# Performance work log

Hardware: AMD Instinct MI355X
Metric: run time of the kernel (lower is better)

Reference implementation:

```python
import jax, jax.numpy as jnp
import numpy as np
from jax import lax

TOP_K = 6
NORM_MIN = 1e-12


def setup_inputs() -> dict:
    key = jax.random.key(0)
    k0, k1, k2, k3, k4, k5 = jax.random.split(key, 6)
    B, S, H, E, I = 2, 1024, 2048, 64, 512
    return {
        "hidden_states": jax.random.normal(k0, (B, S, H), dtype=jnp.float32),
        "gate_w": jax.random.normal(k1, (E, H), dtype=jnp.float32) * 0.02,
        "e_bias": jax.random.normal(k2, (E,), dtype=jnp.float32) * 0.01,
        "gate_proj": jax.random.normal(k3, (E, H, I), dtype=jnp.float32) * 0.02,
        "up_proj": jax.random.normal(k4, (E, H, I), dtype=jnp.float32) * 0.02,
        "down_proj": jax.random.normal(k5, (E, I, H), dtype=jnp.float32) * 0.02,
    }


def reference(hidden_states, gate_w, e_bias, gate_proj, up_proj, down_proj):
    B, S, H = hidden_states.shape
    E = gate_w.shape[0]
    x = hidden_states.reshape(-1, H)                      # [T, H]
    T = x.shape[0]

    # --- routing (done in float32 in the original) ---
    router_logits = x.astype(jnp.float32) @ gate_w.T      # [T, E]
    routing_probs = jax.nn.softmax(router_logits, axis=-1)
    # topk over bias-corrected scores, but weights come from raw probs
    _, selected = lax.top_k(routing_probs + e_bias[None, :], TOP_K)  # [T, k]
    w = jnp.take_along_axis(routing_probs, selected, axis=-1)        # [T, k]
    w = w / jnp.clip(w.sum(axis=-1, keepdims=True), NORM_MIN)
    w = w.astype(hidden_states.dtype)

    # combine weights: [T, E], zero for unselected experts
    combine = jnp.zeros((T, E), dtype=hidden_states.dtype)
    combine = combine.at[jnp.arange(T)[:, None], selected].add(w)

    # --- experts: SwiGLU MLP per expert, weighted-sum combine ---
    def step(acc, params):
        wg, wu, wd, c = params                            # wg,wu [H,I]; wd [I,H]; c [T]
        h = jax.nn.silu(x @ wg) * (x @ wu)                # [T, I]
        return acc + (h @ wd) * c[:, None], None

    init = jnp.zeros((T, H), dtype=hidden_states.dtype)
    final, _ = lax.scan(step, init, (gate_proj, up_proj, down_proj, combine.T))
    return final.reshape(-1), router_logits.reshape(-1)
```

## Files before the change

kernel.cpp:

```cpp
#include <hip/hip_runtime.h>
#include <math.h>

#define T_TOK 2048
#define H_DIM 2048
#define E_NUM 64
#define I_DIM 512
#define TOPK  6
#define NPAIR (T_TOK * TOPK)
#define MAXTILES 80

typedef __attribute__((ext_vector_type(8))) short s8;
typedef __attribute__((ext_vector_type(4))) float f4;
typedef __attribute__((ext_vector_type(8))) unsigned short u16x8;

static __device__ __forceinline__ unsigned short f2bf(float f) {
  unsigned int u = __float_as_uint(f);
  u += 0x7fff + ((u >> 16) & 1);
  return (unsigned short)(u >> 16);
}
static __device__ __forceinline__ unsigned int cvt_pk(float lo, float hi) {
  unsigned int r;
  asm("v_cvt_pk_bf16_f32 %0, %1, %2" : "=v"(r) : "v"(lo), "v"(hi));
  return r;
}
static __device__ __forceinline__ void gload_lds16(const void* g, void* l) {
  __builtin_amdgcn_global_load_lds(
      (const __attribute__((address_space(1))) unsigned int*)g,
      (__attribute__((address_space(3))) unsigned int*)l, 16, 0, 0);
}
#define SBAR()      __builtin_amdgcn_s_barrier()
#define SCHED0()    __builtin_amdgcn_sched_barrier(0)
#define WAIT_LGKM0() asm volatile("s_waitcnt lgkmcnt(0)" ::: "memory")
#define WAIT_VM0()   asm volatile("s_waitcnt vmcnt(0)" ::: "memory")
#define WAIT_VM2()   asm volatile("s_waitcnt vmcnt(2)" ::: "memory")
#define WAIT_VM4()   asm volatile("s_waitcnt vmcnt(4)" ::: "memory")
#define WAIT_VM6()   asm volatile("s_waitcnt vmcnt(6)" ::: "memory")

__global__ __launch_bounds__(512) void router_kernel(
    const float* __restrict__ x, const float* __restrict__ gw,
    const float* __restrict__ ebias, float* __restrict__ logits_out,
    int* __restrict__ sel, float* __restrict__ wsel)
{
  __shared__ float xs[4][H_DIM];
  __shared__ float lg[4][E_NUM];
  int t0 = blockIdx.x * 4;
  int tid = threadIdx.x;
  {
    float4* xsv = (float4*)&xs[0][0];
    const float4* src = (const float4*)(x + (size_t)t0 * H_DIM);
    for (int i = tid; i < 4 * H_DIM / 4; i += 512) xsv[i] = src[i];
  }
  __syncthreads();

  int wave = tid >> 6, lane = tid & 63;
  for (int ii = 0; ii < 4; ++ii) {
    int e0 = wave * 8 + ii * 2, e1 = e0 + 1;
    const float4* g0 = (const float4*)(gw + (size_t)e0 * H_DIM);
    const float4* g1 = (const float4*)(gw + (size_t)e1 * H_DIM);
    float s00=0.f,s01=0.f,s02=0.f,s03=0.f, s10=0.f,s11=0.f,s12=0.f,s13=0.f;
    for (int h4 = lane; h4 < H_DIM / 4; h4 += 64) {
      float4 w0 = g0[h4], w1 = g1[h4];
      float4 a0 = ((const float4*)xs[0])[h4];
      float4 a1 = ((const float4*)xs[1])[h4];
      float4 a2 = ((const float4*)xs[2])[h4];
      float4 a3 = ((const float4*)xs[3])[h4];
      s00 += w0.x*a0.x + w0.y*a0.y + w0.z*a0.z + w0.w*a0.w;
      s01 += w0.x*a1.x + w0.y*a1.y + w0.z*a1.z + w0.w*a1.w;
      s02 += w0.x*a2.x + w0.y*a2.y + w0.z*a2.z + w0.w*a2.w;
      s03 += w0.x*a3.x + w0.y*a3.y + w0.z*a3.z + w0.w*a3.w;
      s10 += w1.x*a0.x + w1.y*a0.y + w1.z*a0.z + w1.w*a0.w;
      s11 += w1.x*a1.x + w1.y*a1.y + w1.z*a1.z + w1.w*a1.w;
      s12 += w1.x*a2.x + w1.y*a2.y + w1.z*a2.z + w1.w*a2.w;
      s13 += w1.x*a3.x + w1.y*a3.y + w1.z*a3.z + w1.w*a3.w;
    }
    for (int off = 32; off; off >>= 1) {
      s00 += __shfl_down(s00, off); s01 += __shfl_down(s01, off);
      s02 += __shfl_down(s02, off); s03 += __shfl_down(s03, off);
      s10 += __shfl_down(s10, off); s11 += __shfl_down(s11, off);
      s12 += __shfl_down(s12, off); s13 += __shfl_down(s13, off);
    }
    if (lane == 0) {
      lg[0][e0]=s00; lg[1][e0]=s01; lg[2][e0]=s02; lg[3][e0]=s03;
      lg[0][e1]=s10; lg[1][e1]=s11; lg[2][e1]=s12; lg[3][e1]=s13;
    }
  }
  __syncthreads();

  if (tid < 256) {
    int tt = tid >> 6, e = tid & 63;
    logits_out[(size_t)(t0 + tt) * E_NUM + e] = lg[tt][e];
  }

  if (wave == 0) {
    for (int tt = 0; tt < 4; ++tt) {
      int t = t0 + tt;
      float v = lg[tt][lane];
      float m = v;
      for (int off = 32; off; off >>= 1) m = fmaxf(m, __shfl_xor(m, off));
      float ex = __expf(v - m);
      float sum = ex;
      for (int off = 32; off; off >>= 1) sum += __shfl_xor(sum, off);
      float prob = ex / sum;
      float sc = prob + ebias[lane];

      int selidx[TOPK]; float selw[TOPK]; float wsum = 0.f;
      #pragma unroll
      for (int k = 0; k < TOPK; ++k) {
        float mm = sc;
        for (int off = 32; off; off >>= 1) mm = fmaxf(mm, __shfl_xor(mm, off));
        unsigned long long ball = __ballot(sc == mm);
        int s = __ffsll(ball) - 1;
        float p = __shfl(prob, s);
        selidx[k] = s; selw[k] = p; wsum += p;
        if (lane == s) sc = -INFINITY;
      }
      if (lane == 0) {
        float inv = 1.f / fmaxf(wsum, 1e-12f);
        #pragma unroll
        for (int k = 0; k < TOPK; ++k) {
          sel[t * TOPK + k] = selidx[k];
          wsel[t * TOPK + k] = selw[k] * inv;
        }
      }
    }
  }
}

__global__ __launch_bounds__(64) void build_lists(
    const int* __restrict__ sel, const float* __restrict__ wsel,
    int* __restrict__ cnt, int* __restrict__ toklist, float* __restrict__ wtlist)
{
  int e = blockIdx.x, lane = threadIdx.x;
  int base = 0;
  for (int t0 = 0; t0 < T_TOK; t0 += 64) {
    int t = t0 + lane;
    int flag = 0; float w = 0.f;
    #pragma unroll
    for (int k = 0; k < TOPK; ++k)
      if (sel[t * TOPK + k] == e) { flag = 1; w = wsel[t * TOPK + k]; }
    unsigned long long b = __ballot(flag);
    int pos = base + __popcll(b & ((1ull << lane) - 1ull));
    if (flag) { toklist[e * T_TOK + pos] = t; wtlist[e * T_TOK + pos] = w; }
    base += __popcll(b);
  }
  if (lane == 0) cnt[e] = base;
}

__global__ void scan_kernel(const int* __restrict__ cnt,
                            int* __restrict__ tmap, int* __restrict__ ntile) {
  if (threadIdx.x == 0) {
    int nt = 0;
    for (int e = 0; e < E_NUM; ++e) {
      int m = (cnt[e] + 255) >> 8;
      for (int tb = 0; tb < m && nt < MAXTILES; ++tb) tmap[nt++] = e * 16 + tb;
    }
    *ntile = nt;
  }
}

__global__ __launch_bounds__(256) void permute_kernel(
    const float* __restrict__ x, const int* __restrict__ cnt,
    const int* __restrict__ toklist, const int* __restrict__ tmap,
    const int* __restrict__ ntile, unsigned short* __restrict__ xt)
{
  int tile = blockIdx.y;
  if (tile >= *ntile) return;
  int ks = blockIdx.x;
  int em = tmap[tile], e = em >> 4, tb = em & 15;
  int n = cnt[e];
  int r = threadIdx.x;
  int tok = toklist[e * T_TOK + min(tb * 256 + r, n - 1)];
  const float4* src = (const float4*)(x + (size_t)tok * H_DIM + ks * 32);
  float4 v[8];
  #pragma unroll
  for (int q = 0; q < 8; ++q) v[q] = src[q];
  int g = (r >> 1) & 3;
  unsigned short* dst = xt + ((size_t)(tile * 64 + ks) * 1024 + r * 4) * 8;
  #pragma unroll
  for (int u = 0; u < 4; ++u) {
    int k16 = u ^ g;
    float4 a = v[2 * k16], b = v[2 * k16 + 1];
    u16x8 p;
    ((unsigned int*)&p)[0] = cvt_pk(a.x, a.y);
    ((unsigned int*)&p)[1] = cvt_pk(a.z, a.w);
    ((unsigned int*)&p)[2] = cvt_pk(b.x, b.y);
    ((unsigned int*)&p)[3] = cvt_pk(b.z, b.w);
    *(u16x8*)(dst + u * 8) = p;
  }
}

__global__ __launch_bounds__(512, 4) void gateup_kernel(
    const unsigned short* __restrict__ xt, const float* __restrict__ gp,
    const float* __restrict__ up, const int* __restrict__ tmap,
    const int* __restrict__ ntile, unsigned short* __restrict__ hat)
{
  __shared__ __align__(16) unsigned short A_lds[2][8192];
  __shared__ __align__(16) unsigned int   Bt[2][2][64 * 20];
  int tile = blockIdx.x;
  if (tile >= *ntile) return;
  int e = tmap[tile] >> 4;
  int ic = blockIdx.y, colbase = ic * 64;
  int tid = threadIdx.x, lane = tid & 63, wave = tid >> 6;
  int matc = wave >> 2, cw = wave & 3;
  int lrow = (lane >> 4) * 4, lcol = lane & 15, kgl = lane >> 4;
  int hp = tid & 15, cb = (tid >> 4) & 15, mstage = tid >> 8;
  const float* bsrc0 = ((mstage == 0) ? gp : up)
      + (size_t)e * (H_DIM * I_DIM) + colbase + (size_t)(2 * hp) * I_DIM + cb * 4;
  const unsigned short* achunk0 = xt + (size_t)tile * 64 * 1024 * 8;

  f4 acc[4][4];
  #pragma unroll
  for (int a = 0; a < 4; ++a)
    #pragma unroll
    for (int b = 0; b < 4; ++b) acc[a][b] = (f4)0.f;

  float4 p0, p1, q0, q1;
  {
    const unsigned short* s = achunk0 + (size_t)(wave * 128 + lane) * 8;
    gload_lds16(s,       &A_lds[0][(wave * 128) * 8]);
    gload_lds16(s + 512, &A_lds[0][(wave * 128 + 64) * 8]);
    p0 = *(const float4*)bsrc0;
    p1 = *(const float4*)(bsrc0 + I_DIM);
    WAIT_VM0();
    unsigned int* db = &Bt[0][mstage][cb * 4 * 20 + hp];
    db[0]  = cvt_pk(p0.x, p1.x); db[20] = cvt_pk(p0.y, p1.y);
    db[40] = cvt_pk(p0.z, p1.z); db[60] = cvt_pk(p0.w, p1.w);
    const float* b1 = bsrc0 + (size_t)32 * I_DIM;
    q0 = *(const float4*)b1;
    q1 = *(const float4*)(b1 + I_DIM);
    WAIT_LGKM0();
    SBAR();
    SCHED0();
  }

#define GU_STEP(K, C0, C1, N0, N1) do {                                            \
    if ((K) + 1 < 64) {                                                            \
      const unsigned short* s = achunk0 + ((size_t)((K) + 1) * 1024 + wave * 128 + lane) * 8; \
      gload_lds16(s,       &A_lds[((K) + 1) & 1][(wave * 128) * 8]);               \
      gload_lds16(s + 512, &A_lds[((K) + 1) & 1][(wave * 128 + 64) * 8]);          \
    }                                                                              \
    if ((K) + 2 < 64) {                                                            \
      const float* b = bsrc0 + (size_t)((K) + 2) * 32 * I_DIM;                     \
      N0 = *(const float4*)b; N1 = *(const float4*)(b + I_DIM);                    \
    }                                                                              \
    if ((K) + 2 < 64)      { WAIT_VM4(); }                                         \
    else if ((K) + 1 < 64) { WAIT_VM2(); }                                         \
    else                   { WAIT_VM0(); }                                         \
    if ((K) + 1 < 64) {                                                            \
      unsigned int* db = &Bt[((K) + 1) & 1][mstage][cb * 4 * 20 + hp];             \
      db[0]  = cvt_pk(C0.x, C1.x); db[20] = cvt_pk(C0.y, C1.y);                    \
      db[40] = cvt_pk(C0.z, C1.z); db[60] = cvt_pk(C0.w, C1.w);                    \
    }                                                                              \
    {                                                                              \
      s8 afr[4];                                                                   \
      _Pragma("unroll")                                                            \
      for (int mf = 0; mf < 4; ++mf) {                                             \
        int r = cw * 64 + mf * 16 + lcol;                                          \
        afr[mf] = *(s8*)&A_lds[(K) & 1][r * 32 + ((kgl ^ ((r >> 1) & 3)) * 8)];    \
      }                                                                            \
      _Pragma("unroll")                                                            \
      for (int nf = 0; nf < 4; ++nf) {                                             \
        s8 bfr = *(s8*)&Bt[(K) & 1][matc][(nf * 16 + lcol) * 20 + kgl * 4];        \
        _Pragma("unroll")                                                          \
        for (int mf = 0; mf < 4; ++mf)                                             \
          acc[mf][nf] = __builtin_amdgcn_mfma_f32_16x16x32_bf16(afr[mf], bfr, acc[mf][nf], 0, 0, 0); \
      }                                                                            \
    }                                                                              \
    if ((K) + 1 < 64) {                                                            \
      if ((K) + 2 < 64) { WAIT_VM2(); } else { WAIT_VM0(); }                       \
      WAIT_LGKM0(); SBAR(); SCHED0();                                              \
    }                                                                              \
  } while (0)

  for (int k = 0; k < 64; k += 2) {
    GU_STEP(k,     q0, q1, p0, p1);
    GU_STEP(k + 1, p0, p1, q0, q1);
  }
#undef GU_STEP

  f4* exch = (f4*)&Bt[0][0][0];
  unsigned short* hs = &A_lds[0][0];
  #pragma unroll
  for (int nf = 0; nf < 4; ++nf) {
    __syncthreads();
    if (wave >= 4) {
      #pragma unroll
      for (int mf = 0; mf < 4; ++mf)
        exch[((wave - 4) * 4 + mf) * 64 + lane] = acc[mf][nf];
    }
    __syncthreads();
    if (wave < 4) {
      #pragma unroll
      for (int mf = 0; mf < 4; ++mf) {
        f4 u = exch[(wave * 4 + mf) * 64 + lane];
        #pragma unroll
        for (int j = 0; j < 4; ++j) {
          float g = acc[mf][nf][j];
          float h = g / (1.f + __expf(-g)) * u[j];
          hs[(wave * 64 + mf * 16 + lrow + j) * 64 + nf * 16 + lcol] = f2bf(h);
        }
      }
    }
  }
  __syncthreads();
  #pragma unroll
  for (int c = 0; c < 2; ++c) {
    unsigned short* base = hat + (size_t)(tile * 16 + ic * 2 + c) * 1024 * 8;
    for (int uu = tid; uu < 1024; uu += 512) {
      int row = uu >> 2, k16 = (uu & 3) ^ ((row >> 1) & 3);
      *(u16x8*)(base + (size_t)uu * 8) = *(const u16x8*)&hs[row * 64 + c * 32 + k16 * 8];
    }
  }
}

__global__ __launch_bounds__(256, 4) void down_kernel(
    const unsigned short* __restrict__ hat, const float* __restrict__ dp,
    const int* __restrict__ cnt, const int* __restrict__ tmap,
    const int* __restrict__ ntile, const int* __restrict__ toklist,
    const float* __restrict__ wtlist, float* __restrict__ out)
{
  __shared__ __align__(16) unsigned short A_lds[2][8192];
  __shared__ __align__(16) unsigned int   Bt[2][64 * 20];
  __shared__ int   stok[256];
  __shared__ float swt[256];
  int tile = blockIdx.x;
  if (tile >= *ntile) return;
  int em = tmap[tile], e = em >> 4, tb = em & 15;
  int n = cnt[e];
  int hc = blockIdx.y, colbase = hc * 64;
  int tid = threadIdx.x, lane = tid & 63, wave = tid >> 6, wbase = wave * 64;
  int lrow = (lane >> 4) * 4, lcol = lane & 15, kgl = lane >> 4;
  int hp = tid & 15, cb = tid >> 4;
  const float* bsrc0 = dp + (size_t)e * (I_DIM * H_DIM) + colbase
                       + (size_t)(2 * hp) * H_DIM + cb * 4;
  const unsigned short* achunk0 = hat + (size_t)tile * 16 * 1024 * 8;

  int rr = tb * 256 + tid;
  stok[tid] = (rr < n) ? toklist[e * T_TOK + rr] : 0;
  swt[tid]  = (rr < n) ? wtlist[e * T_TOK + rr] : 0.f;

  f4 acc[4][4];
  #pragma unroll
  for (int a = 0; a < 4; ++a)
    #pragma unroll
    for (int b = 0; b < 4; ++b) acc[a][b] = (f4)0.f;

  float4 p0, p1, q0, q1;
  {
    const unsigned short* s = achunk0 + (size_t)(wave * 256 + lane) * 8;
    #pragma unroll
    for (int i = 0; i < 4; ++i)
      gload_lds16(s + i * 512, &A_lds[0][(wave * 256 + i * 64) * 8]);
    p0 = *(const float4*)bsrc0;
    p1 = *(const float4*)(bsrc0 + H_DIM);
    WAIT_VM0();
    unsigned int* db = &Bt[0][cb * 4 * 20 + hp];
    db[0]  = cvt_pk(p0.x, p1.x); db[20] = cvt_pk(p0.y, p1.y);
    db[40] = cvt_pk(p0.z, p1.z); db[60] = cvt_pk(p0.w, p1.w);
    const float* b1 = bsrc0 + (size_t)32 * H_DIM;
    q0 = *(const float4*)b1;
    q1 = *(const float4*)(b1 + H_DIM);
    WAIT_LGKM0();
    SBAR();
    SCHED0();
  }

#define DN_STEP(K, C0, C1, N0, N1) do {                                            \
    if ((K) + 1 < 16) {                                                            \
      const unsigned short* s = achunk0 + ((size_t)((K) + 1) * 1024 + wave * 256 + lane) * 8; \
      _Pragma("unroll")                                                            \
      for (int i = 0; i < 4; ++i)                                                  \
        gload_lds16(s + i * 512, &A_lds[((K) + 1) & 1][(wave * 256 + i * 64) * 8]);\
    }                                                                              \
    if ((K) + 2 < 16) {                                                            \
      const float* b = bsrc0 + (size_t)((K) + 2) * 32 * H_DIM;                     \
      N0 = *(const float4*)b; N1 = *(const float4*)(b + H_DIM);                    \
    }                                                                              \
    if ((K) + 2 < 16)      { WAIT_VM6(); }                                         \
    else if ((K) + 1 < 16) { WAIT_VM4(); }                                         \
    else                   { WAIT_VM0(); }                                         \
    if ((K) + 1 < 16) {                                                            \
      unsigned int* db = &Bt[((K) + 1) & 1][cb * 4 * 20 + hp];                     \
      db[0]  = cvt_pk(C0.x, C1.x); db[20] = cvt_pk(C0.y, C1.y);                    \
      db[40] = cvt_pk(C0.z, C1.z); db[60] = cvt_pk(C0.w, C1.w);                    \
    }                                                                              \
    {                                                                              \
      s8 afr[4];                                                                   \
      _Pragma("unroll")                                                            \
      for (int mf = 0; mf < 4; ++mf) {                                             \
        int r = wbase + mf * 16 + lcol;                                            \
        afr[mf] = *(s8*)&A_lds[(K) & 1][r * 32 + ((kgl ^ ((r >> 1) & 3)) * 8)];    \
      }                                                                            \
      _Pragma("unroll")                                                            \
      for (int nf = 0; nf < 4; ++nf) {                                             \
        s8 bfr = *(s8*)&Bt[(K) & 1][(nf * 16 + lcol) * 20 + kgl * 4];              \
        _Pragma("unroll")                                                          \
        for (int mf = 0; mf < 4; ++mf)                                             \
          acc[mf][nf] = __builtin_amdgcn_mfma_f32_16x16x32_bf16(afr[mf], bfr, acc[mf][nf], 0, 0, 0); \
      }                                                                            \
    }                                                                              \
    if ((K) + 1 < 16) {                                                            \
      if ((K) + 2 < 16) { WAIT_VM2(); } else { WAIT_VM0(); }                       \
      WAIT_LGKM0(); SBAR(); SCHED0();                                              \
    }                                                                              \
  } while (0)

  for (int k = 0; k < 16; k += 2) {
    DN_STEP(k,     q0, q1, p0, p1);
    DN_STEP(k + 1, p0, p1, q0, q1);
  }
#undef DN_STEP

  #pragma unroll
  for (int mf = 0; mf < 4; ++mf)
    #pragma unroll
    for (int nf = 0; nf < 4; ++nf)
      #pragma unroll
      for (int j = 0; j < 4; ++j) {
        int r = wbase + mf * 16 + lrow + j;
        if (tb * 256 + r < n)
          atomicAdd(&out[(size_t)stok[r] * H_DIM + colbase + nf * 16 + lcol],
                    acc[mf][nf][j] * swt[r]);
      }
}

extern "C" void kernel_launch(void* const* d_in, const int* in_sizes, int n_in,
                              void* d_out, int out_size, void* d_ws, size_t ws_size,
                              hipStream_t stream) {
  const float* hidden = (const float*)d_in[0];
  const float* gate_w = (const float*)d_in[1];
  const float* e_bias = (const float*)d_in[2];
  const float* gate_p = (const float*)d_in[3];
  const float* up_p   = (const float*)d_in[4];
  const float* down_p = (const float*)d_in[5];

  float* out_final  = (float*)d_out;
  float* out_logits = out_final + (size_t)T_TOK * H_DIM;

  int*   cnt     = (int*)d_ws;
  int*   texp    = cnt + 64;
  int*   ntile   = texp + 64;
  int*   tmap    = ntile + 16;
  int*   sel     = tmap + MAXTILES;
  float* wsel    = (float*)(sel + NPAIR);
  int*   toklist = (int*)(wsel + NPAIR);
  float* wtlist  = (float*)(toklist + E_NUM * T_TOK);
  unsigned short* xt  = (unsigned short*)(wtlist + E_NUM * T_TOK);
  unsigned short* hat = xt + (size_t)MAXTILES * 64 * 1024 * 8;

  hipMemsetAsync(out_final, 0, (size_t)T_TOK * H_DIM * sizeof(float), stream);

  router_kernel<<<T_TOK / 4, 512, 0, stream>>>(hidden, gate_w, e_bias, out_logits, sel, wsel);
  build_lists<<<E_NUM, 64, 0, stream>>>(sel, wsel, cnt, toklist, wtlist);
  scan_kernel<<<1, 64, 0, stream>>>(cnt, tmap, ntile);
  permute_kernel<<<dim3(64, MAXTILES), 256, 0, stream>>>(hidden, cnt, toklist, tmap, ntile, xt);
  gateup_kernel<<<dim3(MAXTILES, I_DIM / 64), 512, 0, stream>>>(
      xt, gate_p, up_p, tmap, ntile, hat);
  down_kernel<<<dim3(MAXTILES, H_DIM / 64), 256, 0, stream>>>(
      hat, down_p, cnt, tmap, ntile, toklist, wtlist, out_final);
}
```

Measured before the change: 569.4 us.

## Replace atomic scatter-add in down projection with bf16 partials plus gather-reduce

The down kernel now writes weighted per-(token,expert) results as bf16 rows into a partial buffer (reusing the xt workspace) instead of atomically adding fp32 values into the output. A new reduce kernel gathers each token's six partial rows through a position map built during list construction and writes the output directly, so the output memset is no longer needed. This removes contended global atomics and replaces them with coalesced stores and one extra kernel. In exchange, the partial results are rounded to bf16 before they are summed, which costs some accuracy.

```diff
diff --git a/kernel.cpp b/kernel.cpp
--- a/kernel.cpp
+++ b/kernel.cpp
@@ -128,29 +128,35 @@
 
 __global__ __launch_bounds__(64) void build_lists(
     const int* __restrict__ sel, const float* __restrict__ wsel,
-    int* __restrict__ cnt, int* __restrict__ toklist, float* __restrict__ wtlist)
+    int* __restrict__ cnt, int* __restrict__ toklist, float* __restrict__ wtlist,
+    int* __restrict__ posmap)
 {
   int e = blockIdx.x, lane = threadIdx.x;
   int base = 0;
   for (int t0 = 0; t0 < T_TOK; t0 += 64) {
     int t = t0 + lane;
-    int flag = 0; float w = 0.f;
+    int flag = 0, kk = 0; float w = 0.f;
     #pragma unroll
     for (int k = 0; k < TOPK; ++k)
-      if (sel[t * TOPK + k] == e) { flag = 1; w = wsel[t * TOPK + k]; }
+      if (sel[t * TOPK + k] == e) { flag = 1; kk = k; w = wsel[t * TOPK + k]; }
     unsigned long long b = __ballot(flag);
     int pos = base + __popcll(b & ((1ull << lane) - 1ull));
-    if (flag) { toklist[e * T_TOK + pos] = t; wtlist[e * T_TOK + pos] = w; }
+    if (flag) {
+      toklist[e * T_TOK + pos] = t;
+      wtlist[e * T_TOK + pos] = w;
+      posmap[t * TOPK + kk] = pos;
+    }
     base += __popcll(b);
   }
   if (lane == 0) cnt[e] = base;
 }
 
-__global__ void scan_kernel(const int* __restrict__ cnt,
+__global__ void scan_kernel(const int* __restrict__ cnt, int* __restrict__ texp,
                             int* __restrict__ tmap, int* __restrict__ ntile) {
   if (threadIdx.x == 0) {
     int nt = 0;
     for (int e = 0; e < E_NUM; ++e) {
+      texp[e] = nt;
       int m = (cnt[e] + 255) >> 8;
       for (int tb = 0; tb < m && nt < MAXTILES; ++tb) tmap[nt++] = e * 16 + tb;
     }
@@ -316,12 +322,11 @@
 __global__ __launch_bounds__(256, 4) void down_kernel(
     const unsigned short* __restrict__ hat, const float* __restrict__ dp,
     const int* __restrict__ cnt, const int* __restrict__ tmap,
-    const int* __restrict__ ntile, const int* __restrict__ toklist,
-    const float* __restrict__ wtlist, float* __restrict__ out)
+    const int* __restrict__ ntile, const float* __restrict__ wtlist,
+    unsigned short* __restrict__ pout)
 {
   __shared__ __align__(16) unsigned short A_lds[2][8192];
   __shared__ __align__(16) unsigned int   Bt[2][64 * 20];
-  __shared__ int   stok[256];
   __shared__ float swt[256];
   int tile = blockIdx.x;
   if (tile >= *ntile) return;
@@ -336,8 +341,7 @@
   const unsigned short* achunk0 = hat + (size_t)tile * 16 * 1024 * 8;
 
   int rr = tb * 256 + tid;
-  stok[tid] = (rr < n) ? toklist[e * T_TOK + rr] : 0;
-  swt[tid]  = (rr < n) ? wtlist[e * T_TOK + rr] : 0.f;
+  swt[tid] = (rr < n) ? wtlist[e * T_TOK + rr] : 0.f;
 
   f4 acc[4][4];
   #pragma unroll
@@ -411,6 +415,8 @@
   }
 #undef DN_STEP
 
+  __syncthreads();
+  unsigned short* hs = &A_lds[0][0];
   #pragma unroll
   for (int mf = 0; mf < 4; ++mf)
     #pragma unroll
@@ -418,10 +424,39 @@
       #pragma unroll
       for (int j = 0; j < 4; ++j) {
         int r = wbase + mf * 16 + lrow + j;
-        if (tb * 256 + r < n)
-          atomicAdd(&out[(size_t)stok[r] * H_DIM + colbase + nf * 16 + lcol],
-                    acc[mf][nf][j] * swt[r]);
+        hs[r * 64 + nf * 16 + lcol] = f2bf(acc[mf][nf][j] * swt[r]);
       }
+  __syncthreads();
+  for (int u = tid; u < 2048; u += 256) {
+    int row = u >> 3, unit = u & 7;
+    *(u16x8*)(pout + (size_t)(tile * 256 + row) * H_DIM + colbase + unit * 8) =
+        *(const u16x8*)&hs[row * 64 + unit * 8];
+  }
+}
+
+__global__ __launch_bounds__(256) void reduce_kernel(
+    const unsigned short* __restrict__ pout, const int* __restrict__ sel,
+    const int* __restrict__ posmap, const int* __restrict__ texp,
+    float* __restrict__ out)
+{
+  int t = blockIdx.x, tid = threadIdx.x;
+  int col = tid * 8;
+  float acc[8];
+  #pragma unroll
+  for (int j = 0; j < 8; ++j) acc[j] = 0.f;
+  #pragma unroll
+  for (int k = 0; k < TOPK; ++k) {
+    int e = sel[t * TOPK + k];
+    int row = texp[e] * 256 + posmap[t * TOPK + k];
+    u16x8 v = *(const u16x8*)(pout + (size_t)row * H_DIM + col);
+    #pragma unroll
+    for (int j = 0; j < 8; ++j)
+      acc[j] += __uint_as_float((unsigned int)(unsigned short)v[j] << 16);
+  }
+  float4 o0 = {acc[0], acc[1], acc[2], acc[3]};
+  float4 o1 = {acc[4], acc[5], acc[6], acc[7]};
+  *(float4*)(out + (size_t)t * H_DIM + col)     = o0;
+  *(float4*)(out + (size_t)t * H_DIM + col + 4) = o1;
 }
 
 extern "C" void kernel_launch(void* const* d_in, const int* in_sizes, int n_in,
@@ -443,19 +478,20 @@
   int*   tmap    = ntile + 16;
   int*   sel     = tmap + MAXTILES;
   float* wsel    = (float*)(sel + NPAIR);
-  int*   toklist = (int*)(wsel + NPAIR);
+  int*   posmap  = (int*)(wsel + NPAIR);
+  int*   toklist = posmap + NPAIR;
   float* wtlist  = (float*)(toklist + E_NUM * T_TOK);
   unsigned short* xt  = (unsigned short*)(wtlist + E_NUM * T_TOK);
   unsigned short* hat = xt + (size_t)MAXTILES * 64 * 1024 * 8;
-
-  hipMemsetAsync(out_final, 0, (size_t)T_TOK * H_DIM * sizeof(float), stream);
+  unsigned short* pout = xt;
 
   router_kernel<<<T_TOK / 4, 512, 0, stream>>>(hidden, gate_w, e_bias, out_logits, sel, wsel);
-  build_lists<<<E_NUM, 64, 0, stream>>>(sel, wsel, cnt, toklist, wtlist);
-  scan_kernel<<<1, 64, 0, stream>>>(cnt, tmap, ntile);
+  build_lists<<<E_NUM, 64, 0, stream>>>(sel, wsel, cnt, toklist, wtlist, posmap);
+  scan_kernel<<<1, 64, 0, stream>>>(cnt, texp, tmap, ntile);
   permute_kernel<<<dim3(64, MAXTILES), 256, 0, stream>>>(hidden, cnt, toklist, tmap, ntile, xt);
   gateup_kernel<<<dim3(MAXTILES, I_DIM / 64), 512, 0, stream>>>(
       xt, gate_p, up_p, tmap, ntile, hat);
   down_kernel<<<dim3(MAXTILES, H_DIM / 64), 256, 0, stream>>>(
-      hat, down_p, cnt, tmap, ntile, toklist, wtlist, out_final);
-}
+      hat, down_p, cnt, tmap, ntile, wtlist, pout);
+  reduce_kernel<<<T_TOK, 256, 0, stream>>>(pout, sel, posmap, texp, out_final);
+}
```

After: 536.2 us. -5.8%, faster.
